# Optimization experiments

Measured on AMD Instinct MI355X. Metric: run time of the kernel, lower is better.

## Reference

```python
import jax, jax.numpy as jnp
import numpy as np
import math

H_HEAD = 8
D_MODEL = 1024
DEPTH = 12
D_K = D_MODEL // H_HEAD // 2  # 64
LAMBDA_INIT = 0.8 - 0.6 * math.exp(-0.3 * DEPTH)
EPS = 1e-5


def setup_inputs() -> dict:
    key = jax.random.key(0)
    ks = jax.random.split(key, 16)
    B, S, D = 2, 2048, D_MODEL
    std = 1.0 / math.sqrt(D)
    inp = {
        "query": jax.random.normal(ks[0], (B, S, D), jnp.float32),
        "key":   jax.random.normal(ks[1], (B, S, D), jnp.float32),
        "value": jax.random.normal(ks[2], (B, S, D), jnp.float32),
        "wq_w": jax.random.normal(ks[3], (D, D), jnp.float32) * std,
        "wq_b": jnp.zeros((D,), jnp.float32),
        "wk_w": jax.random.normal(ks[4], (D, D), jnp.float32) * std,
        "wk_b": jnp.zeros((D,), jnp.float32),
        "wv_w": jax.random.normal(ks[5], (D, D), jnp.float32) * std,
        "wv_b": jnp.zeros((D,), jnp.float32),
        "fc_w": jax.random.normal(ks[6], (D, D), jnp.float32) * std,
        "fc_b": jnp.zeros((D,), jnp.float32),
        "lambda_q1": jax.random.normal(ks[7], (D_K,), jnp.float32) * 0.1,
        "lambda_k1": jax.random.normal(ks[8], (D_K,), jnp.float32) * 0.1,
        "lambda_q2": jax.random.normal(ks[9], (D_K,), jnp.float32) * 0.1,
        "lambda_k2": jax.random.normal(ks[10], (D_K,), jnp.float32) * 0.1,
        "subln_w": jnp.ones((2 * D_K,), jnp.float32),
    }
    return inp


def _rms_norm(x, w):
    xf = x.astype(jnp.float32)
    out = xf * jax.lax.rsqrt(jnp.mean(xf * xf, axis=-1, keepdims=True) + EPS)
    return out.astype(x.dtype) * w


def reference(query, key, value, wq_w, wq_b, wk_w, wk_b, wv_w, wv_b,
              fc_w, fc_b, lambda_q1, lambda_k1, lambda_q2, lambda_k2, subln_w):
    B, S, D = query.shape
    h, dk = H_HEAD, D_K
    # projections (torch Linear: x @ W^T + b)
    q = (query @ wq_w.T + wq_b).reshape(B, S, 2 * h, dk).transpose(0, 2, 1, 3)   # [B,2h,S,dk]
    k = (key   @ wk_w.T + wk_b).reshape(B, S, 2 * h, dk).transpose(0, 2, 1, 3)   # [B,2h,S,dk]
    v = (value @ wv_w.T + wv_b).reshape(B, S, h, 2 * dk).transpose(0, 2, 1, 3)   # [B,h,S,2dk]

    scores = jnp.einsum('bhqd,bhkd->bhqk', q, k) / math.sqrt(dk)                 # [B,2h,S,S]
    aw = jax.nn.softmax(scores.astype(jnp.float32), axis=-1).astype(scores.dtype)

    lam1 = jnp.exp(jnp.sum(lambda_q1 * lambda_k1).astype(jnp.float32)).astype(q.dtype)
    lam2 = jnp.exp(jnp.sum(lambda_q2 * lambda_k2).astype(jnp.float32)).astype(q.dtype)
    lam = lam1 - lam2 + LAMBDA_INIT

    aw = aw.reshape(B, h, 2, S, S)
    aw = aw[:, :, 0] - lam * aw[:, :, 1]                                          # [B,h,S,S]

    attn = jnp.einsum('bhqk,bhkd->bhqd', aw, v)                                   # [B,h,S,2dk]
    attn = _rms_norm(attn, subln_w) * (1.0 - LAMBDA_INIT)
    attn = attn.transpose(0, 2, 1, 3).reshape(B, S, h * 2 * dk)
    out = attn @ fc_w.T + fc_b
    return (out, aw)
```

## Files before the change

### kernel.cpp

```cpp
#include <hip/hip_runtime.h>
#include <stdint.h>

#define DEV __device__ __forceinline__

typedef short s8v __attribute__((ext_vector_type(8)));
typedef short s4v __attribute__((ext_vector_type(4)));
typedef float f4v __attribute__((ext_vector_type(4)));
typedef unsigned short u16;

static constexpr float LAMBDA_INIT = 0.783605766531624464f;
static constexpr float OUT_SCALE   = 0.216394233468375536f;

DEV u16 f2bf(float f) {
    uint32_t u = __builtin_bit_cast(uint32_t, f);
    u += 0x7fffu + ((u >> 16) & 1u);
    return (u16)(u >> 16);
}
DEV float bf2f(u16 v) {
    return __builtin_bit_cast(float, (uint32_t)v << 16);
}

__global__ __launch_bounds__(256)
void cvt_kernel(const float* __restrict__ q, const float* __restrict__ k,
                const float* __restrict__ v, const float* __restrict__ w0,
                const float* __restrict__ w1, const float* __restrict__ w2,
                const float* __restrict__ w3,
                u16* qo, u16* ko, u16* vo, u16* o0, u16* o1, u16* o2, u16* o3)
{
    int bid = blockIdx.x;
    const float* src; u16* dst; int base;
    if      (bid < 2048) { src = q;  dst = qo; base = bid * 2048; }
    else if (bid < 4096) { src = k;  dst = ko; base = (bid - 2048) * 2048; }
    else if (bid < 6144) { src = v;  dst = vo; base = (bid - 4096) * 2048; }
    else if (bid < 6656) { src = w0; dst = o0; base = (bid - 6144) * 2048; }
    else if (bid < 7168) { src = w1; dst = o1; base = (bid - 6656) * 2048; }
    else if (bid < 7680) { src = w2; dst = o2; base = (bid - 7168) * 2048; }
    else                 { src = w3; dst = o3; base = (bid - 7680) * 2048; }
    int i = base + threadIdx.x * 8;
    float4 a = *(const float4*)(src + i);
    float4 b = *(const float4*)(src + i + 4);
    u16 r[8] = { f2bf(a.x), f2bf(a.y), f2bf(a.z), f2bf(a.w),
                 f2bf(b.x), f2bf(b.y), f2bf(b.z), f2bf(b.w) };
    *(s8v*)(dst + i) = *(const s8v*)r;
}

template<int OUT_MODE>
__global__ __launch_bounds__(256)
void gemm128(const u16* __restrict__ A, const u16* __restrict__ W,
             const float* __restrict__ bias, void* __restrict__ Cp)
{
    constexpr int K = 1024;
    __shared__ __align__(16) char smem[OUT_MODE == 2 ? 32768 : 24576];
    const int m0 = blockIdx.x * 128, n0 = blockIdx.y * 64;
    const int t = threadIdx.x, lane = t & 63, wave = t >> 6;
    const int l15 = lane & 15, g = lane >> 4;

    f4v acc[2][4] = {};

    for (int k0 = 0; k0 < K; k0 += 64) {
#pragma unroll
        for (int i = 0; i < 4; ++i) {
            int idx = t + i * 256, row = idx >> 3, piece = idx & 7;
            s8v v = *(const s8v*)(A + (size_t)(m0 + row) * K + k0 + piece * 8);
            *(s8v*)(smem + row * 128 + ((piece * 16) ^ ((row & 7) << 4))) = v;
        }
#pragma unroll
        for (int i = 0; i < 2; ++i) {
            int idx = t + i * 256, row = idx >> 3, piece = idx & 7;
            s8v v = *(const s8v*)(W + (size_t)(n0 + row) * K + k0 + piece * 8);
            *(s8v*)(smem + 16384 + row * 128 + ((piece * 16) ^ ((row & 7) << 4))) = v;
        }
        __syncthreads();
#pragma unroll
        for (int ks = 0; ks < 2; ++ks) {
            s8v af[2], bf4[4];
#pragma unroll
            for (int mt = 0; mt < 2; ++mt) {
                int row = wave * 32 + mt * 16 + l15;
                af[mt] = *(const s8v*)(smem + row * 128 + ((ks * 64 + g * 16) ^ ((l15 & 7) << 4)));
            }
#pragma unroll
            for (int nt = 0; nt < 4; ++nt) {
                int row = nt * 16 + l15;
                bf4[nt] = *(const s8v*)(smem + 16384 + row * 128 + ((ks * 64 + g * 16) ^ ((l15 & 7) << 4)));
            }
#pragma unroll
            for (int mt = 0; mt < 2; ++mt)
#pragma unroll
                for (int nt = 0; nt < 4; ++nt)
                    acc[mt][nt] = __builtin_amdgcn_mfma_f32_16x16x32_bf16(af[mt], bf4[nt], acc[mt][nt], 0, 0, 0);
        }
        __syncthreads();
    }

    float bv[4];
#pragma unroll
    for (int nt = 0; nt < 4; ++nt) bv[nt] = bias[n0 + nt * 16 + l15];

    if (OUT_MODE == 0) {
        u16* rep = (u16*)smem;
#pragma unroll
        for (int mt = 0; mt < 2; ++mt)
#pragma unroll
            for (int nt = 0; nt < 4; ++nt)
#pragma unroll
                for (int r = 0; r < 4; ++r)
                    rep[(wave * 32 + mt * 16 + g * 4 + r) * 64 + nt * 16 + l15] = f2bf(acc[mt][nt][r] + bv[nt]);
        __syncthreads();
        u16* C = (u16*)Cp;
#pragma unroll
        for (int j = 0; j < 4; ++j) {
            int m = j * 32 + (t >> 3), chunk = t & 7;
            s8v v = *(const s8v*)(smem + m * 128 + chunk * 16);
            *(s8v*)(C + (size_t)(m0 + m) * 1024 + n0 + chunk * 8) = v;
        }
    } else if (OUT_MODE == 1) {
        u16* LT = (u16*)smem;
#pragma unroll
        for (int mt = 0; mt < 2; ++mt)
#pragma unroll
            for (int nt = 0; nt < 4; ++nt)
#pragma unroll
                for (int r = 0; r < 4; ++r)
                    LT[(nt * 16 + l15) * 136 + wave * 32 + mt * 16 + g * 4 + r] = f2bf(acc[mt][nt][r] + bv[nt]);
        __syncthreads();
        u16* C = (u16*)Cp;
        const int b = m0 >> 11, s0 = m0 & 2047;
#pragma unroll
        for (int j = 0; j < 4; ++j) {
            int n = j * 16 + (t >> 4), chunk = t & 15;
            s8v v = *(const s8v*)(smem + n * 272 + chunk * 16);
            *(s8v*)(C + ((size_t)b * 1024 + n0 + n) * 2048 + s0 + chunk * 8) = v;
        }
    } else {
        float* rep = (float*)smem;
#pragma unroll
        for (int mt = 0; mt < 2; ++mt)
#pragma unroll
            for (int nt = 0; nt < 4; ++nt)
#pragma unroll
                for (int r = 0; r < 4; ++r)
                    rep[(wave * 32 + mt * 16 + g * 4 + r) * 64 + nt * 16 + l15] = acc[mt][nt][r] + bv[nt];
        __syncthreads();
        float* C = (float*)Cp;
#pragma unroll
        for (int j = 0; j < 8; ++j) {
            int m = j * 16 + (t >> 4), c4 = t & 15;
            float4 v = *(const float4*)(smem + m * 256 + c4 * 16);
            *(float4*)(C + (size_t)(m0 + m) * 1024 + n0 + c4 * 4) = v;
        }
    }
}

__global__ __launch_bounds__(256, 4)
void attn_sum(const u16* __restrict__ Qb, const u16* __restrict__ Kb,
              float* __restrict__ psum)
{
    constexpr int S = 2048, D = 1024;
    __shared__ __align__(16) char smem[32768];
    const int bid0 = blockIdx.x;
    const int bid = (bid0 & 7) * 256 + (bid0 >> 3);
    const int sl = bid & 3, qt = (bid >> 2) & 31, h = (bid >> 7) & 7, b = bid >> 10;
    const int t = threadIdx.x, lane = t & 63, qw = t >> 6;
    const int l15 = lane & 15, g = lane >> 4;
    const int wrow0 = qt * 64 + qw * 16;

    const u16* Qbase = Qb + ((size_t)b * S + wrow0 + l15) * D + h * 128;
    s8v q1[2], q2[2];
#pragma unroll
    for (int ks = 0; ks < 2; ++ks) {
        q1[ks] = *(const s8v*)(Qbase + ks * 32 + g * 8);
        q2[ks] = *(const s8v*)(Qbase + 64 + ks * 32 + g * 8);
    }
    const u16* Ksrc = Kb + (size_t)b * S * D + (size_t)(sl * 512) * D + h * 128;
    const int swz = (l15 & 7) << 4;

    float t1a[4] = {}, t2a[4] = {};
    s8v kreg[4];
#pragma unroll
    for (int i = 0; i < 4; ++i) {
        int idx = t + i * 256, row = idx >> 4, piece = idx & 15;
        kreg[i] = *(const s8v*)(Ksrc + (size_t)row * D + piece * 8);
    }
#pragma unroll
    for (int i = 0; i < 4; ++i) {
        int idx = t + i * 256, row = idx >> 4, piece = idx & 15;
        int sub = piece >> 3, colB = (piece & 7) * 16;
        *(s8v*)(smem + sub * 8192 + row * 128 + (colB ^ ((row & 7) << 4))) = kreg[i];
    }
#pragma unroll
    for (int i = 0; i < 4; ++i) {
        int idx = t + i * 256, row = idx >> 4, piece = idx & 15;
        kreg[i] = *(const s8v*)(Ksrc + (size_t)(64 + row) * D + piece * 8);
    }
    __syncthreads();

    for (int kt = 0; kt < 8; ++kt) {
        char* cur = smem + (kt & 1) * 16384;
        char* nxt = smem + ((kt + 1) & 1) * 16384;
        if (kt < 7) {
#pragma unroll
            for (int i = 0; i < 4; ++i) {
                int idx = t + i * 256, row = idx >> 4, piece = idx & 15;
                int sub = piece >> 3, colB = (piece & 7) * 16;
                *(s8v*)(nxt + sub * 8192 + row * 128 + (colB ^ ((row & 7) << 4))) = kreg[i];
            }
        }
        if (kt < 6) {
            const u16* src = Ksrc + (size_t)(kt + 2) * 64 * D;
#pragma unroll
            for (int i = 0; i < 4; ++i) {
                int idx = t + i * 256, row = idx >> 4, piece = idx & 15;
                kreg[i] = *(const s8v*)(src + (size_t)row * D + piece * 8);
            }
        }
        f4v s1[4] = {}, s2[4] = {};
        __builtin_amdgcn_s_setprio(1);
#pragma unroll
        for (int nt = 0; nt < 4; ++nt)
#pragma unroll
            for (int ks = 0; ks < 2; ++ks) {
                int ro = (nt * 16 + l15) * 128 + ((ks * 64 + g * 16) ^ swz);
                s1[nt] = __builtin_amdgcn_mfma_f32_16x16x32_bf16(q1[ks], *(const s8v*)(cur + ro), s1[nt], 0, 0, 0);
                s2[nt] = __builtin_amdgcn_mfma_f32_16x16x32_bf16(q2[ks], *(const s8v*)(cur + 8192 + ro), s2[nt], 0, 0, 0);
            }
        __builtin_amdgcn_s_setprio(0);
#pragma unroll
        for (int nt = 0; nt < 4; ++nt)
#pragma unroll
            for (int r = 0; r < 4; ++r) {
                t1a[r] += __expf(s1[nt][r] * 0.125f);
                t2a[r] += __expf(s2[nt][r] * 0.125f);
            }
        __syncthreads();
    }

#pragma unroll
    for (int r = 0; r < 4; ++r) {
#pragma unroll
        for (int off = 1; off < 16; off <<= 1) {
            t1a[r] += __shfl_xor(t1a[r], off);
            t2a[r] += __shfl_xor(t2a[r], off);
        }
    }
    if (l15 == 0) {
        float* pp = psum + (size_t)(((b * 8 + h) * 2048) + wrow0 + g * 4) * 8;
#pragma unroll
        for (int r = 0; r < 4; ++r) {
            pp[r * 8 + sl]     = t1a[r];
            pp[r * 8 + 4 + sl] = t2a[r];
        }
    }
}

__global__ __launch_bounds__(512, 4)
void attn_kernel(const u16* __restrict__ Qb, const u16* __restrict__ Kb,
                 const u16* __restrict__ Vt, const float* __restrict__ psum,
                 const float* __restrict__ lq1, const float* __restrict__ lk1,
                 const float* __restrict__ lq2, const float* __restrict__ lk2,
                 const float* __restrict__ subw, float* __restrict__ aw,
                 u16* __restrict__ an)
{
    constexpr int S = 2048, D = 1024;
    __shared__ __align__(16) char smem[74752];
    const int bid0 = blockIdx.x;
    const int bid = (bid0 & 7) * 64 + (bid0 >> 3);
    const int qt = bid & 31, h = (bid >> 5) & 7, b = bid >> 8;
    const int t = threadIdx.x, lane = t & 63, w = t >> 6;
    const int qw = w >> 1, kw = w & 1;
    const int l15 = lane & 15, g = lane >> 4;
    const int qrow0 = qt * 64, wrow0 = qrow0 + qw * 16;

    short* P  = (short*)(smem + 65536);
    float* Po = (float*)smem;

    float lam;
    {
        float p1 = lq1[lane] * lk1[lane], p2 = lq2[lane] * lk2[lane];
#pragma unroll
        for (int off = 1; off < 64; off <<= 1) {
            p1 += __shfl_xor(p1, off);
            p2 += __shfl_xor(p2, off);
        }
        lam = expf(p1) - expf(p2) + LAMBDA_INIT;
    }

    const u16* Qbase = Qb + ((size_t)b * S + wrow0 + l15) * D + h * 128;
    s8v q1[2], q2[2];
#pragma unroll
    for (int ks = 0; ks < 2; ++ks) {
        q1[ks] = *(const s8v*)(Qbase + ks * 32 + g * 8);
        q2[ks] = *(const s8v*)(Qbase + 64 + ks * 32 + g * 8);
    }
    const u16* Ksrc = Kb + (size_t)b * S * D + h * 128;
    const u16* Vsrc = Vt + ((size_t)b * 1024 + h * 128) * 2048;
    const int swz = (l15 & 7) << 4;

    float il1[4], il2[4];
    {
        const float* pp = psum + (size_t)(((b * 8 + h) * 2048) + wrow0 + g * 4) * 8;
#pragma unroll
        for (int r = 0; r < 4; ++r) {
            float4 a = *(const float4*)(pp + r * 8);
            float4 c = *(const float4*)(pp + r * 8 + 4);
            il1[r] = 1.f / ((a.x + a.y) + (a.z + a.w));
            il2[r] = 1.f / ((c.x + c.y) + (c.z + c.w));
        }
    }

    s8v kreg[2], vreg[2];
#pragma unroll
    for (int i = 0; i < 2; ++i) {
        int idx = t + i * 512;
        { int row = idx >> 4, piece = idx & 15;
          kreg[i] = *(const s8v*)(Ksrc + (size_t)row * D + piece * 8); }
        { int dd = idx >> 3, piece = idx & 7;
          vreg[i] = *(const s8v*)(Vsrc + (size_t)dd * 2048 + piece * 8); }
    }
#pragma unroll
    for (int i = 0; i < 2; ++i) {
        int idx = t + i * 512;
        { int row = idx >> 4, piece = idx & 15;
          int sub = piece >> 3, colB = (piece & 7) * 16;
          *(s8v*)(smem + sub * 8192 + row * 128 + (colB ^ ((row & 7) << 4))) = kreg[i]; }
        { int dd = idx >> 3, piece = idx & 7;
          *(s8v*)(smem + 16384 + dd * 128 + ((piece * 16) ^ ((dd & 7) << 4))) = vreg[i]; }
    }
#pragma unroll
    for (int i = 0; i < 2; ++i) {
        int idx = t + i * 512;
        { int row = idx >> 4, piece = idx & 15;
          kreg[i] = *(const s8v*)(Ksrc + (size_t)(64 + row) * D + piece * 8); }
        { int dd = idx >> 3, piece = idx & 7;
          vreg[i] = *(const s8v*)(Vsrc + (size_t)dd * 2048 + 64 + piece * 8); }
    }
    __syncthreads();

    f4v po[8] = {};
    float* awb = aw + ((size_t)(b * 8 + h) * S + qrow0) * S;
    const int drl = lane >> 3;
    const int dc4 = (lane & 7) * 4;

    for (int kt = 0; kt < 32; ++kt) {
        const int kv0 = kt * 64;
        char* cur = smem + (kt & 1) * 32768;
        char* nxt = smem + ((kt + 1) & 1) * 32768;
        if (kt < 31) {
#pragma unroll
            for (int i = 0; i < 2; ++i) {
                int idx = t + i * 512;
                { int row = idx >> 4, piece = idx & 15;
                  int sub = piece >> 3, colB = (piece & 7) * 16;
                  *(s8v*)(nxt + sub * 8192 + row * 128 + (colB ^ ((row & 7) << 4))) = kreg[i]; }
                { int dd = idx >> 3, piece = idx & 7;
                  *(s8v*)(nxt + 16384 + dd * 128 + ((piece * 16) ^ ((dd & 7) << 4))) = vreg[i]; }
            }
        }
        if (kt < 30) {
            const u16* ksp = Ksrc + (size_t)(kv0 + 128) * D;
            const u16* vsp = Vsrc + kv0 + 128;
#pragma unroll
            for (int i = 0; i < 2; ++i) {
                int idx = t + i * 512;
                { int row = idx >> 4, piece = idx & 15;
                  kreg[i] = *(const s8v*)(ksp + (size_t)row * D + piece * 8); }
                { int dd = idx >> 3, piece = idx & 7;
                  vreg[i] = *(const s8v*)(vsp + (size_t)dd * 2048 + piece * 8); }
            }
        }

        f4v s1[2] = {}, s2[2] = {};
        __builtin_amdgcn_s_setprio(1);
#pragma unroll
        for (int nt = 0; nt < 2; ++nt)
#pragma unroll
            for (int ks = 0; ks < 2; ++ks) {
                int ro = (kw * 32 + nt * 16 + l15) * 128 + ((ks * 64 + g * 16) ^ swz);
                s1[nt] = __builtin_amdgcn_mfma_f32_16x16x32_bf16(q1[ks], *(const s8v*)(cur + ro), s1[nt], 0, 0, 0);
                s2[nt] = __builtin_amdgcn_mfma_f32_16x16x32_bf16(q2[ks], *(const s8v*)(cur + 8192 + ro), s2[nt], 0, 0, 0);
            }
        __builtin_amdgcn_s_setprio(0);
#pragma unroll
        for (int nt = 0; nt < 2; ++nt)
#pragma unroll
            for (int r = 0; r < 4; ++r) {
                float p1 = __expf(s1[nt][r] * 0.125f) * il1[r];
                float p2 = __expf(s2[nt][r] * 0.125f) * il2[r];
                P[(qw * 16 + g * 4 + r) * 72 + kw * 32 + nt * 16 + l15] = (short)f2bf(p1 - lam * p2);
            }

#pragma unroll
        for (int half = 0; half < 2; ++half) {
            int row = qw * 16 + half * 8 + drl;
            s4v pv = *(const s4v*)(P + row * 72 + kw * 32 + dc4);
            f4v o = { bf2f((u16)pv.x), bf2f((u16)pv.y), bf2f((u16)pv.z), bf2f((u16)pv.w) };
            __builtin_nontemporal_store(o, (f4v*)(awb + (size_t)row * S + kv0 + kw * 32 + dc4));
        }

        s8v pf = *(const s8v*)(P + (qw * 16 + l15) * 72 + kw * 32 + g * 8);
        __builtin_amdgcn_s_setprio(1);
#pragma unroll
        for (int dn = 0; dn < 8; ++dn) {
            const s8v* vf = (const s8v*)(cur + 16384 + (dn * 16 + l15) * 128 + ((kw * 64 + g * 16) ^ swz));
            po[dn] = __builtin_amdgcn_mfma_f32_16x16x32_bf16(pf, *vf, po[dn], 0, 0, 0);
        }
        __builtin_amdgcn_s_setprio(0);
        __syncthreads();
    }

    if (kw == 0) {
#pragma unroll
        for (int dn = 0; dn < 8; ++dn)
#pragma unroll
            for (int r = 0; r < 4; ++r)
                Po[(qw * 16 + g * 4 + r) * 128 + dn * 16 + l15] = po[dn][r];
    }
    __syncthreads();
    if (kw == 1) {
#pragma unroll
        for (int dn = 0; dn < 8; ++dn)
#pragma unroll
            for (int r = 0; r < 4; ++r)
                Po[(qw * 16 + g * 4 + r) * 128 + dn * 16 + l15] += po[dn][r];
    }
    __syncthreads();

    {
        const int row = t >> 3, c0 = (t & 7) * 16;
        float ss = 0.f;
#pragma unroll
        for (int j = 0; j < 4; ++j) {
            float4 v4 = *(const float4*)(Po + row * 128 + c0 + j * 4);
            ss += v4.x * v4.x + v4.y * v4.y + v4.z * v4.z + v4.w * v4.w;
        }
#pragma unroll
        for (int off = 1; off < 8; off <<= 1) ss += __shfl_xor(ss, off);
        float rs = rsqrtf(ss * (1.0f / 128.0f) + 1e-5f) * OUT_SCALE;
        u16* dst = an + ((size_t)b * S + qrow0 + row) * D + h * 128;
#pragma unroll
        for (int j = 0; j < 2; ++j) {
            u16 tmp[8];
#pragma unroll
            for (int e = 0; e < 8; ++e) {
                int c = c0 + j * 8 + e;
                tmp[e] = f2bf(Po[row * 128 + c] * rs * subw[c]);
            }
            *(s8v*)(dst + c0 + j * 8) = *(const s8v*)tmp;
        }
    }
}

extern "C" void kernel_launch(void* const* d_in, const int* in_sizes, int n_in,
                              void* d_out, int out_size, void* d_ws, size_t ws_size,
                              hipStream_t stream)
{
    const float* query = (const float*)d_in[0];
    const float* key   = (const float*)d_in[1];
    const float* value = (const float*)d_in[2];
    const float* wq_w  = (const float*)d_in[3];
    const float* wq_b  = (const float*)d_in[4];
    const float* wk_w  = (const float*)d_in[5];
    const float* wk_b  = (const float*)d_in[6];
    const float* wv_w  = (const float*)d_in[7];
    const float* wv_b  = (const float*)d_in[8];
    const float* fc_w  = (const float*)d_in[9];
    const float* fc_b  = (const float*)d_in[10];
    const float* lq1   = (const float*)d_in[11];
    const float* lk1   = (const float*)d_in[12];
    const float* lq2   = (const float*)d_in[13];
    const float* lk2   = (const float*)d_in[14];
    const float* subw  = (const float*)d_in[15];

    const size_t MB = 1024 * 1024;
    char* ws = (char*)d_ws;
    u16*   Qbf = (u16*)(ws);
    u16*   Kbf = (u16*)(ws + 8 * MB);
    u16*   Vtg = (u16*)(ws + 16 * MB);
    u16*   ANb = (u16*)(ws + 24 * MB);
    u16*   wqb = (u16*)(ws + 32 * MB);
    u16*   wkb = (u16*)(ws + 34 * MB);
    u16*   wvb = (u16*)(ws + 36 * MB);
    u16*   fcb = (u16*)(ws + 38 * MB);
    float* psum = (float*)(ws + 32 * MB);

    float* out0 = (float*)d_out;
    float* awp  = out0 + (size_t)4096 * 1024;
    u16* qx = (u16*)awp;
    u16* kx = qx + (size_t)4096 * 1024;
    u16* vx = kx + (size_t)4096 * 1024;

    cvt_kernel<<<dim3(8192), dim3(256), 0, stream>>>(query, key, value, wq_w, wk_w, wv_w, fc_w,
                                                     qx, kx, vx, wqb, wkb, wvb, fcb);
    dim3 grid(32, 16), blk(256);
    gemm128<0><<<grid, blk, 0, stream>>>(qx, wqb, wq_b, Qbf);
    gemm128<0><<<grid, blk, 0, stream>>>(kx, wkb, wk_b, Kbf);
    gemm128<1><<<grid, blk, 0, stream>>>(vx, wvb, wv_b, Vtg);
    attn_sum<<<dim3(2048), dim3(256), 0, stream>>>(Qbf, Kbf, psum);
    attn_kernel<<<dim3(512), dim3(512), 0, stream>>>(Qbf, Kbf, Vtg, psum, lq1, lk1, lq2, lk2,
                                                     subw, awp, ANb);
    gemm128<2><<<grid, blk, 0, stream>>>(ANb, fcb, fc_b, out0);
}
```

Before: 190.4 us.

## Enlarge projection GEMM tiles, use packed bf16 conversion and exp2 softmax

The projection and output GEMMs move from 128x64 tiles with 256 threads to 128x128 tiles with 512 threads (8 waves in a 4x2 grid). This halves the number of blocks and reuses each A tile across more columns, and the fp32 output epilogue is staged in two halves to fit shared memory. Separately, the fp32-to-bf16 conversions switch to the hardware v_cvt_pk_bf16_f32 instruction, and the softmax exponentials use exp2f with a prescaled constant instead of __expf. The larger tiles cut grid parallelism to 256 blocks, which may underfill the GPU's CUs.

```diff
diff --git a/kernel.cpp b/kernel.cpp
--- a/kernel.cpp
+++ b/kernel.cpp
@@ -6,10 +6,12 @@
 typedef short s8v __attribute__((ext_vector_type(8)));
 typedef short s4v __attribute__((ext_vector_type(4)));
 typedef float f4v __attribute__((ext_vector_type(4)));
+typedef uint32_t u32x4 __attribute__((ext_vector_type(4)));
 typedef unsigned short u16;
 
 static constexpr float LAMBDA_INIT = 0.783605766531624464f;
 static constexpr float OUT_SCALE   = 0.216394233468375536f;
+static constexpr float SC_EXP2     = 0.18033688011112042f;
 
 DEV u16 f2bf(float f) {
     uint32_t u = __builtin_bit_cast(uint32_t, f);
@@ -18,6 +20,11 @@
 }
 DEV float bf2f(u16 v) {
     return __builtin_bit_cast(float, (uint32_t)v << 16);
+}
+DEV uint32_t cvtpk(float lo, float hi) {
+    uint32_t r;
+    asm("v_cvt_pk_bf16_f32 %0, %1, %2" : "=v"(r) : "v"(lo), "v"(hi));
+    return r;
 }
 
 __global__ __launch_bounds__(256)
@@ -39,51 +46,48 @@
     int i = base + threadIdx.x * 8;
     float4 a = *(const float4*)(src + i);
     float4 b = *(const float4*)(src + i + 4);
-    u16 r[8] = { f2bf(a.x), f2bf(a.y), f2bf(a.z), f2bf(a.w),
-                 f2bf(b.x), f2bf(b.y), f2bf(b.z), f2bf(b.w) };
-    *(s8v*)(dst + i) = *(const s8v*)r;
+    u32x4 pk = { cvtpk(a.x, a.y), cvtpk(a.z, a.w), cvtpk(b.x, b.y), cvtpk(b.z, b.w) };
+    *(u32x4*)(dst + i) = pk;
 }
 
 template<int OUT_MODE>
-__global__ __launch_bounds__(256)
-void gemm128(const u16* __restrict__ A, const u16* __restrict__ W,
+__global__ __launch_bounds__(512)
+void gemmBig(const u16* __restrict__ A, const u16* __restrict__ W,
              const float* __restrict__ bias, void* __restrict__ Cp)
 {
     constexpr int K = 1024;
-    __shared__ __align__(16) char smem[OUT_MODE == 2 ? 32768 : 24576];
-    const int m0 = blockIdx.x * 128, n0 = blockIdx.y * 64;
-    const int t = threadIdx.x, lane = t & 63, wave = t >> 6;
+    __shared__ __align__(16) char smem[OUT_MODE == 1 ? 34816 : 32768];
+    const int m0 = blockIdx.x * 128, n0 = blockIdx.y * 128;
+    const int t = threadIdx.x, lane = t & 63, w = t >> 6;
+    const int wm = w & 3, wn = w >> 2;
     const int l15 = lane & 15, g = lane >> 4;
 
     f4v acc[2][4] = {};
 
     for (int k0 = 0; k0 < K; k0 += 64) {
 #pragma unroll
-        for (int i = 0; i < 4; ++i) {
-            int idx = t + i * 256, row = idx >> 3, piece = idx & 7;
+        for (int i = 0; i < 2; ++i) {
+            int idx = t + i * 512, row = idx >> 3, piece = idx & 7;
             s8v v = *(const s8v*)(A + (size_t)(m0 + row) * K + k0 + piece * 8);
             *(s8v*)(smem + row * 128 + ((piece * 16) ^ ((row & 7) << 4))) = v;
         }
 #pragma unroll
         for (int i = 0; i < 2; ++i) {
-            int idx = t + i * 256, row = idx >> 3, piece = idx & 7;
+            int idx = t + i * 512, row = idx >> 3, piece = idx & 7;
             s8v v = *(const s8v*)(W + (size_t)(n0 + row) * K + k0 + piece * 8);
             *(s8v*)(smem + 16384 + row * 128 + ((piece * 16) ^ ((row & 7) << 4))) = v;
         }
         __syncthreads();
 #pragma unroll
         for (int ks = 0; ks < 2; ++ks) {
+            const int cswz = (ks * 64 + g * 16) ^ ((l15 & 7) << 4);
             s8v af[2], bf4[4];
 #pragma unroll
-            for (int mt = 0; mt < 2; ++mt) {
-                int row = wave * 32 + mt * 16 + l15;
-                af[mt] = *(const s8v*)(smem + row * 128 + ((ks * 64 + g * 16) ^ ((l15 & 7) << 4)));
-            }
-#pragma unroll
-            for (int nt = 0; nt < 4; ++nt) {
-                int row = nt * 16 + l15;
-                bf4[nt] = *(const s8v*)(smem + 16384 + row * 128 + ((ks * 64 + g * 16) ^ ((l15 & 7) << 4)));
-            }
+            for (int mt = 0; mt < 2; ++mt)
+                af[mt] = *(const s8v*)(smem + (wm * 32 + mt * 16 + l15) * 128 + cswz);
+#pragma unroll
+            for (int nt = 0; nt < 4; ++nt)
+                bf4[nt] = *(const s8v*)(smem + 16384 + (wn * 64 + nt * 16 + l15) * 128 + cswz);
 #pragma unroll
             for (int mt = 0; mt < 2; ++mt)
 #pragma unroll
@@ -95,7 +99,7 @@
 
     float bv[4];
 #pragma unroll
-    for (int nt = 0; nt < 4; ++nt) bv[nt] = bias[n0 + nt * 16 + l15];
+    for (int nt = 0; nt < 4; ++nt) bv[nt] = bias[n0 + wn * 64 + nt * 16 + l15];
 
     if (OUT_MODE == 0) {
         u16* rep = (u16*)smem;
@@ -105,14 +109,14 @@
             for (int nt = 0; nt < 4; ++nt)
 #pragma unroll
                 for (int r = 0; r < 4; ++r)
-                    rep[(wave * 32 + mt * 16 + g * 4 + r) * 64 + nt * 16 + l15] = f2bf(acc[mt][nt][r] + bv[nt]);
+                    rep[(wm * 32 + mt * 16 + g * 4 + r) * 128 + wn * 64 + nt * 16 + l15] = f2bf(acc[mt][nt][r] + bv[nt]);
         __syncthreads();
         u16* C = (u16*)Cp;
+        int row = t >> 2, cb = (t & 3) * 32;
 #pragma unroll
         for (int j = 0; j < 4; ++j) {
-            int m = j * 32 + (t >> 3), chunk = t & 7;
-            s8v v = *(const s8v*)(smem + m * 128 + chunk * 16);
-            *(s8v*)(C + (size_t)(m0 + m) * 1024 + n0 + chunk * 8) = v;
+            s8v v = *(const s8v*)(smem + row * 256 + cb * 2 + j * 16);
+            *(s8v*)(C + (size_t)(m0 + row) * 1024 + n0 + cb + j * 8) = v;
         }
     } else if (OUT_MODE == 1) {
         u16* LT = (u16*)smem;
@@ -122,32 +126,38 @@
             for (int nt = 0; nt < 4; ++nt)
 #pragma unroll
                 for (int r = 0; r < 4; ++r)
-                    LT[(nt * 16 + l15) * 136 + wave * 32 + mt * 16 + g * 4 + r] = f2bf(acc[mt][nt][r] + bv[nt]);
+                    LT[(wn * 64 + nt * 16 + l15) * 136 + wm * 32 + mt * 16 + g * 4 + r] = f2bf(acc[mt][nt][r] + bv[nt]);
         __syncthreads();
         u16* C = (u16*)Cp;
         const int b = m0 >> 11, s0 = m0 & 2047;
+        int n = t >> 2, cb = (t & 3) * 32;
 #pragma unroll
         for (int j = 0; j < 4; ++j) {
-            int n = j * 16 + (t >> 4), chunk = t & 15;
-            s8v v = *(const s8v*)(smem + n * 272 + chunk * 16);
-            *(s8v*)(C + ((size_t)b * 1024 + n0 + n) * 2048 + s0 + chunk * 8) = v;
+            s8v v = *(const s8v*)(smem + n * 272 + cb * 2 + j * 16);
+            *(s8v*)(C + ((size_t)b * 1024 + n0 + n) * 2048 + s0 + cb + j * 8) = v;
         }
     } else {
         float* rep = (float*)smem;
-#pragma unroll
-        for (int mt = 0; mt < 2; ++mt)
-#pragma unroll
-            for (int nt = 0; nt < 4; ++nt)
-#pragma unroll
-                for (int r = 0; r < 4; ++r)
-                    rep[(wave * 32 + mt * 16 + g * 4 + r) * 64 + nt * 16 + l15] = acc[mt][nt][r] + bv[nt];
-        __syncthreads();
         float* C = (float*)Cp;
 #pragma unroll
-        for (int j = 0; j < 8; ++j) {
-            int m = j * 16 + (t >> 4), c4 = t & 15;
-            float4 v = *(const float4*)(smem + m * 256 + c4 * 16);
-            *(float4*)(C + (size_t)(m0 + m) * 1024 + n0 + c4 * 4) = v;
+        for (int p = 0; p < 2; ++p) {
+            if ((wm >> 1) == p) {
+#pragma unroll
+                for (int mt = 0; mt < 2; ++mt)
+#pragma unroll
+                    for (int nt = 0; nt < 4; ++nt)
+#pragma unroll
+                        for (int r = 0; r < 4; ++r)
+                            rep[((wm & 1) * 32 + mt * 16 + g * 4 + r) * 128 + wn * 64 + nt * 16 + l15] = acc[mt][nt][r] + bv[nt];
+            }
+            __syncthreads();
+            int lrow = t >> 3, c0 = (t & 7) * 16;
+#pragma unroll
+            for (int j = 0; j < 4; ++j) {
+                float4 v = *(const float4*)(rep + lrow * 128 + c0 + j * 4);
+                *(float4*)(C + (size_t)(m0 + p * 64 + lrow) * 1024 + n0 + c0 + j * 4) = v;
+            }
+            __syncthreads();
         }
     }
 }
@@ -229,8 +239,8 @@
         for (int nt = 0; nt < 4; ++nt)
 #pragma unroll
             for (int r = 0; r < 4; ++r) {
-                t1a[r] += __expf(s1[nt][r] * 0.125f);
-                t2a[r] += __expf(s2[nt][r] * 0.125f);
+                t1a[r] += exp2f(s1[nt][r] * SC_EXP2);
+                t2a[r] += exp2f(s2[nt][r] * SC_EXP2);
             }
         __syncthreads();
     }
@@ -381,13 +391,14 @@
             }
         __builtin_amdgcn_s_setprio(0);
 #pragma unroll
-        for (int nt = 0; nt < 2; ++nt)
-#pragma unroll
-            for (int r = 0; r < 4; ++r) {
-                float p1 = __expf(s1[nt][r] * 0.125f) * il1[r];
-                float p2 = __expf(s2[nt][r] * 0.125f) * il2[r];
-                P[(qw * 16 + g * 4 + r) * 72 + kw * 32 + nt * 16 + l15] = (short)f2bf(p1 - lam * p2);
-            }
+        for (int r = 0; r < 4; ++r) {
+            float va = exp2f(s1[0][r] * SC_EXP2) * il1[r] - lam * (exp2f(s2[0][r] * SC_EXP2) * il2[r]);
+            float vb = exp2f(s1[1][r] * SC_EXP2) * il1[r] - lam * (exp2f(s2[1][r] * SC_EXP2) * il2[r]);
+            uint32_t pk = cvtpk(va, vb);
+            short* pb = P + (qw * 16 + g * 4 + r) * 72 + kw * 32 + l15;
+            pb[0]  = (short)(u16)pk;
+            pb[16] = (short)(u16)(pk >> 16);
+        }
 
 #pragma unroll
         for (int half = 0; half < 2; ++half) {
@@ -491,12 +502,12 @@
 
     cvt_kernel<<<dim3(8192), dim3(256), 0, stream>>>(query, key, value, wq_w, wk_w, wv_w, fc_w,
                                                      qx, kx, vx, wqb, wkb, wvb, fcb);
-    dim3 grid(32, 16), blk(256);
-    gemm128<0><<<grid, blk, 0, stream>>>(qx, wqb, wq_b, Qbf);
-    gemm128<0><<<grid, blk, 0, stream>>>(kx, wkb, wk_b, Kbf);
-    gemm128<1><<<grid, blk, 0, stream>>>(vx, wvb, wv_b, Vtg);
+    dim3 grid(32, 8), blk(512);
+    gemmBig<0><<<grid, blk, 0, stream>>>(qx, wqb, wq_b, Qbf);
+    gemmBig<0><<<grid, blk, 0, stream>>>(kx, wkb, wk_b, Kbf);
+    gemmBig<1><<<grid, blk, 0, stream>>>(vx, wvb, wv_b, Vtg);
     attn_sum<<<dim3(2048), dim3(256), 0, stream>>>(Qbf, Kbf, psum);
     attn_kernel<<<dim3(512), dim3(512), 0, stream>>>(Qbf, Kbf, Vtg, psum, lq1, lk1, lq2, lk2,
                                                      subw, awp, ANb);
-    gemm128<2><<<grid, blk, 0, stream>>>(ANb, fcb, fc_b, out0);
-}
+    gemmBig<2><<<grid, blk, 0, stream>>>(ANb, fcb, fc_b, out0);
+}
```

Result: slower. 217.6 us (+14.3%).
